# Performance work log

Hardware: AMD Instinct MI355X
Metric: run time of the kernel (lower is better)

## Reference

```python
import jax, jax.numpy as jnp
import numpy as np

E = 4      # num_ensemble
DIN = 256  # input_dim
D = 256    # d_model (output_dim)
B = 16
T = 1024
LN_EPS = 1e-5


def setup_inputs() -> dict:
    key = jax.random.key(0)
    ks = jax.random.split(key, 14)
    s = 0.02
    x = jax.random.normal(ks[0], (B, T, DIN), dtype=jnp.float32)
    in_proj_w = s * jax.random.normal(ks[1], (3, E, DIN, D), dtype=jnp.float32)
    in_proj_b = jnp.zeros((3, E, D), dtype=jnp.float32)
    mid_w = s * jax.random.normal(ks[2], (2, E, D, D), dtype=jnp.float32)
    mid_b = jnp.zeros((2, E, D), dtype=jnp.float32)
    ff_w1 = s * jax.random.normal(ks[3], (E, D, D), dtype=jnp.float32)
    ff_b1 = jnp.zeros((E, D), dtype=jnp.float32)
    ff_w2 = s * jax.random.normal(ks[4], (E, D, D), dtype=jnp.float32)
    ff_b2 = jnp.zeros((E, D), dtype=jnp.float32)
    ln_w = jnp.ones((E, D), dtype=jnp.float32)
    ln_b = jnp.zeros((E, D), dtype=jnp.float32)
    # LRU initializer (r_min=0.9, r_max=0.999)
    r_min, r_max = 0.9, 0.999
    u1 = jax.random.uniform(ks[5], (E, D), dtype=jnp.float32)
    u2 = jax.random.uniform(ks[6], (E, D), dtype=jnp.float32)
    nu_log = jnp.log(-0.5 * jnp.log(u1 * (r_max ** 2 - r_min ** 2) + r_min ** 2))
    theta_log = jnp.log(u2 * 2.0 * np.pi)
    # |lambda|^2 = exp(-2*exp(nu_log))
    gamma_log = jnp.log(jnp.sqrt(1.0 - jnp.exp(-2.0 * jnp.exp(nu_log))))
    params_log = jnp.stack([nu_log, theta_log, gamma_log], axis=0)  # (3,E,D)
    return {"x": x, "in_proj_w": in_proj_w, "in_proj_b": in_proj_b,
            "params_log": params_log, "mid_w": mid_w, "mid_b": mid_b,
            "ff_w1": ff_w1, "ff_b1": ff_b1, "ff_w2": ff_w2, "ff_b2": ff_b2,
            "ln_w": ln_w, "ln_b": ln_b}


def _forward(x, in_proj_w, in_proj_b, params_log, mid_w, mid_b,
             ff_w1, ff_b1, ff_w2, ff_b2, ln_w, ln_b):
    # in_proj: 3 ensemble linears -> u: (3, E, B, T, D)
    u = jnp.einsum('bti,keio->kebto', x, in_proj_w) + in_proj_b[:, :, None, None, :]
    input_real, input_imag, o = u[0], u[1], u[2]

    params = jnp.exp(params_log)           # (3,E,D)
    nu, theta, gamma = params[0], params[1], params[2]
    mag = jnp.exp(-nu)
    f_real = mag * jnp.cos(theta)          # (E,D)
    f_imag = mag * jnp.sin(theta)

    ir = gamma[:, None, None, :] * input_real  # (E,B,T,D)
    ii = gamma[:, None, None, :] * input_imag

    # complex linear recurrence h_t = f * h_{t-1} + u_t over time axis
    fr = f_real[:, None, :]                # (E,1,D) broadcast over B
    fi = f_imag[:, None, :]
    ir_t = jnp.moveaxis(ir, 2, 0)          # (T,E,B,D)
    ii_t = jnp.moveaxis(ii, 2, 0)

    def step(carry, ut):
        hr, hi = carry
        ur, ui = ut
        hr2 = fr * hr - fi * hi + ur
        hi2 = fr * hi + fi * hr + ui
        return (hr2, hi2), (hr2, hi2)

    h0 = (jnp.zeros((E, B, D), x.dtype), jnp.zeros((E, B, D), x.dtype))
    (hr_last, hi_last), (out_r_t, out_i_t) = jax.lax.scan(step, h0, (ir_t, ii_t))
    output_real = jnp.moveaxis(out_r_t, 0, 2)  # (E,B,T,D)
    output_imag = jnp.moveaxis(out_i_t, 0, 2)

    # hidden packing: (1, B, 2*E*D) with ensemble blocks concatenated, real then imag
    hr_pack = jnp.transpose(hr_last, (1, 0, 2)).reshape(B, E * D)
    hi_pack = jnp.transpose(hi_last, (1, 0, 2)).reshape(B, E * D)
    hidden = jnp.concatenate([hr_pack, hi_pack], axis=-1)[None]  # (1,B,2ED)

    # middle_proj: 2 ensemble linears applied to (real, imag)
    stacked = jnp.stack([output_real, output_imag], axis=0)  # (2,E,B,T,D)
    mid = jnp.einsum('kebtd,kedo->kebto', stacked, mid_w) + mid_b[:, :, None, None, :]
    out = mid[0] - mid[1] + o                                # (E,B,T,D)

    # EnsemblePositionWiseFeedForward (dropout=0 -> identity)
    h1 = jax.nn.gelu(jnp.einsum('ebtd,edo->ebto', out, ff_w1)
                     + ff_b1[:, None, None, :], approximate=False)
    h2 = jnp.einsum('ebtd,edo->ebto', h1, ff_w2) + ff_b2[:, None, None, :] + out
    # LayerNorm over joint (E, D) dims for each (b, t)
    mean = jnp.mean(h2, axis=(0, 3), keepdims=True)
    var = jnp.var(h2, axis=(0, 3), keepdims=True)
    out_ln = (h2 - mean) / jnp.sqrt(var + LN_EPS)
    out_ln = out_ln * ln_w[:, None, None, :] + ln_b[:, None, None, :]
    return out_ln, hidden


def reference(x, in_proj_w, in_proj_b, params_log, mid_w, mid_b,
              ff_w1, ff_b1, ff_w2, ff_b2, ln_w, ln_b):
    return _forward(x, in_proj_w, in_proj_b, params_log, mid_w, mid_b,
                    ff_w1, ff_b1, ff_w2, ff_b2, ln_w, ln_b)
```

## Files before the change

### kernel.cpp

```cpp
#include <hip/hip_runtime.h>
#include <stdint.h>

#define BT_ 16384
#define TT  1024
#define CHUNKS 32
#define CLEN   32
#define LANES  16384

typedef __bf16 bf16x8 __attribute__((ext_vector_type(8)));
typedef float  f32x4  __attribute__((ext_vector_type(4)));
typedef unsigned int u32x4 __attribute__((ext_vector_type(4)));
typedef unsigned short u16;

__device__ __forceinline__ float b2f(u16 s){
    union { float f; unsigned int u; } c; c.u = ((unsigned int)s) << 16; return c.f;
}
__device__ __forceinline__ u16 f2b(float f){
    union { float f; unsigned int u; } c; c.f = f;
    unsigned int u = c.u;
    return (u16)((u + 0x7fffu + ((u >> 16) & 1u)) >> 16);
}

__device__ __forceinline__ void gload_lds16(const u16* g, u16* lds){
    __builtin_amdgcn_global_load_lds(
        (const __attribute__((address_space(1))) void*)g,
        (__attribute__((address_space(3))) void*)lds, 16, 0, 0);
}

__global__ __launch_bounds__(256) void conv_k(const float* __restrict__ x, u16* __restrict__ xc)
{
    long i = ((long)blockIdx.x * 256 + threadIdx.x) * 8;
    float4 v0 = *reinterpret_cast<const float4*>(x + i);
    float4 v1 = *reinterpret_cast<const float4*>(x + i + 4);
    union { u16 s[8]; u32x4 v; } p;
    p.s[0] = f2b(v0.x); p.s[1] = f2b(v0.y); p.s[2] = f2b(v0.z); p.s[3] = f2b(v0.w);
    p.s[4] = f2b(v1.x); p.s[5] = f2b(v1.y); p.s[6] = f2b(v1.z); p.s[7] = f2b(v1.w);
    *reinterpret_cast<u32x4*>(xc + i) = p.v;
}

__global__ __launch_bounds__(256) void prep_w(
    const float* __restrict__ ipw, const float* __restrict__ mw,
    const float* __restrict__ fw1, const float* __restrict__ fw2,
    u16* __restrict__ d_ipw, u16* __restrict__ d_mw,
    u16* __restrict__ d_fw1, u16* __restrict__ d_fw2)
{
    __shared__ u16 tile[64][72];
    int blk = blockIdx.x;
    int w = blk >> 4, t = blk & 15;
    int tr = (t >> 2) * 64;
    int tc = (t & 3) * 64;
    const float* src; u16* dst; int ostride; float sign = 1.f;
    if (w < 12)      { src = ipw + (size_t)w * 65536; dst = d_ipw + (size_t)w * 65536; ostride = 256; }
    else if (w < 20) { int u = w - 12, c = u >> 2, e = u & 3;
                       src = mw + (size_t)u * 65536;
                       dst = d_mw + (size_t)e * 131072 + c * 256; ostride = 512;
                       if (c) sign = -1.f; }
    else if (w < 24) { int e = w - 20; src = fw1 + (size_t)e * 65536; dst = d_fw1 + (size_t)e * 65536; ostride = 256; }
    else             { int e = w - 24; src = fw2 + (size_t)e * 65536; dst = d_fw2 + (size_t)e * 65536; ostride = 256; }

    int q = threadIdx.x;
    int r = q >> 2, cb = (q & 3) * 16;
#pragma unroll
    for (int j = 0; j < 4; j++) {
        int col = cb + j * 4;
        const float4 v = *reinterpret_cast<const float4*>(src + (size_t)(tr + r) * 256 + tc + col);
        tile[r][col + 0] = f2b(v.x * sign);
        tile[r][col + 1] = f2b(v.y * sign);
        tile[r][col + 2] = f2b(v.z * sign);
        tile[r][col + 3] = f2b(v.w * sign);
    }
    __syncthreads();
    int ol = q >> 2, ib = (q & 3) * 16;
    union { u16 s[8]; u32x4 v; } p0, p1;
#pragma unroll
    for (int k = 0; k < 8; k++) { p0.s[k] = tile[ib + k][ol]; p1.s[k] = tile[ib + 8 + k][ol]; }
    u16* drow = dst + (size_t)(tc + ol) * ostride + tr + ib;
    *reinterpret_cast<u32x4*>(drow)     = p0.v;
    *reinterpret_cast<u32x4*>(drow + 8) = p1.v;
}

__global__ __launch_bounds__(256, 3) void gemm_k(
    const u16* __restrict__ A0, const u16* __restrict__ B0,
    const float* __restrict__ biasf, const u16* __restrict__ aux,
    const float* __restrict__ gamlogf, u16* __restrict__ out0,
    u16* __restrict__ out1, int K, int mode, int MT)
{
    __shared__ __align__(16) u16 Bs[64 * 256];
    __shared__ __align__(16) float fs_all[4][1024];

    int tid  = threadIdx.x;
    int wave = tid >> 6, lane = tid & 63;
    int quad = lane >> 4, l16 = lane & 15;
    int n0 = blockIdx.y * 64;
    int z = blockIdx.z;
    int e, k3 = 0;
    const u16* A;
    const u16* Bm;
    if (mode == 1) { k3 = z >> 2; e = z & 3; A = A0; }
    else           { e = z; A = A0 + (size_t)e * BT_ * K; }
    Bm = B0 + (size_t)(mode == 1 ? z : e) * 256 * K;

    int srow = lane >> 5, schunk = lane & 31;
    int nhalf = K >> 8;

    float bias_nf[4], gam_nf[4];
#pragma unroll
    for (int nf = 0; nf < 4; nf++) {
        int col = n0 + nf * 16 + l16;
        if (mode == 1) {
            bias_nf[nf] = biasf[z * 256 + col];
            gam_nf[nf] = (k3 < 2) ? expf(gamlogf[2048 + e * 256 + col]) : 1.f;
        } else if (mode == 2) {
            bias_nf[nf] = biasf[e * 256 + col] - biasf[1024 + e * 256 + col];
        } else {
            bias_nf[nf] = biasf[e * 256 + col];
        }
    }

    float* fs = fs_all[wave];
    int rr = lane >> 3, ch = lane & 7;

    for (int mt = 0; mt < MT; mt++) {
        int m0 = (blockIdx.x * MT + mt) * 256;

        f32x4 acc[4][4];
#pragma unroll
        for (int i = 0; i < 4; i++)
#pragma unroll
            for (int j = 0; j < 4; j++) acc[i][j] = (f32x4){0.f, 0.f, 0.f, 0.f};

        for (int kh = 0; kh < nhalf; kh++) {
            if (nhalf > 1 || mt == 0) {
                if (mt || kh) __syncthreads();
#pragma unroll
                for (int i = 0; i < 8; i++) {
                    int row = wave * 16 + i * 2 + srow;
                    int c = schunk ^ (row & 7);
                    gload_lds16(Bm + (size_t)(n0 + row) * K + kh * 256 + c * 8,
                                &Bs[(wave * 16 + i * 2) * 256]);
                }
                __syncthreads();
            }

            const u16* Ar0 = A + (size_t)(m0 + wave * 64 + l16) * K + kh * 256 + quad * 8;
            const u16* Ar1 = Ar0 + (size_t)16 * K;
            const u16* Ar2 = Ar0 + (size_t)32 * K;
            const u16* Ar3 = Ar0 + (size_t)48 * K;

            bf16x8 ac0, ac1, ac2, ac3, an0, an1, an2, an3;
            { union { u32x4 v; bf16x8 b; } u;
              u.v = *reinterpret_cast<const u32x4*>(Ar0); ac0 = u.b;
              u.v = *reinterpret_cast<const u32x4*>(Ar1); ac1 = u.b;
              u.v = *reinterpret_cast<const u32x4*>(Ar2); ac2 = u.b;
              u.v = *reinterpret_cast<const u32x4*>(Ar3); ac3 = u.b; }
#pragma unroll
            for (int kt = 0; kt < 8; kt++) {
                if (kt < 7) {
                    union { u32x4 v; bf16x8 b; } u;
                    u.v = *reinterpret_cast<const u32x4*>(Ar0 + (kt + 1) * 32); an0 = u.b;
                    u.v = *reinterpret_cast<const u32x4*>(Ar1 + (kt + 1) * 32); an1 = u.b;
                    u.v = *reinterpret_cast<const u32x4*>(Ar2 + (kt + 1) * 32); an2 = u.b;
                    u.v = *reinterpret_cast<const u32x4*>(Ar3 + (kt + 1) * 32); an3 = u.b;
                }
#pragma unroll
                for (int nf = 0; nf < 4; nf++) {
                    int row = nf * 16 + l16;
                    int c = (kt * 4 + quad) ^ (row & 7);
                    union { u32x4 v; bf16x8 b; } u;
                    u.v = *reinterpret_cast<const u32x4*>(&Bs[row * 256 + c * 8]);
                    acc[0][nf] = __builtin_amdgcn_mfma_f32_16x16x32_bf16(ac0, u.b, acc[0][nf], 0, 0, 0);
                    acc[1][nf] = __builtin_amdgcn_mfma_f32_16x16x32_bf16(ac1, u.b, acc[1][nf], 0, 0, 0);
                    acc[2][nf] = __builtin_amdgcn_mfma_f32_16x16x32_bf16(ac2, u.b, acc[2][nf], 0, 0, 0);
                    acc[3][nf] = __builtin_amdgcn_mfma_f32_16x16x32_bf16(ac3, u.b, acc[3][nf], 0, 0, 0);
                }
                ac0 = an0; ac1 = an1; ac2 = an2; ac3 = an3;
            }
        }

#pragma unroll
        for (int s = 0; s < 4; s++) {
#pragma unroll
            for (int nf = 0; nf < 4; nf++) {
                int colsw = (nf * 16 + l16) ^ (quad * 8);
#pragma unroll
                for (int r = 0; r < 4; r++) {
                    float v = acc[s][nf][r] + bias_nf[nf];
                    if (mode == 1) v *= gam_nf[nf];
                    if (mode == 3) v = 0.5f * v * (1.0f + erff(v * 0.70710678118654752f));
                    fs[(quad * 4 + r) * 64 + colsw] = v;
                }
            }
#pragma unroll
            for (int i = 0; i < 2; i++) {
                int rl = i * 8 + rr;
                int grow = m0 + wave * 64 + s * 16 + rl;
                const float* sp = fs + rl * 64 + ((ch * 8) ^ ((rl >> 2) * 8));
                f32x4 v0 = *reinterpret_cast<const f32x4*>(sp);
                f32x4 v1 = *reinterpret_cast<const f32x4*>(sp + 4);
                float w[8] = { v0[0], v0[1], v0[2], v0[3], v1[0], v1[1], v1[2], v1[3] };
                u16* dstp;
                if (mode == 1) {
                    if (k3 < 2) dstp = out0 + (((size_t)(e * BT_ + grow)) * 2 + k3) * 256 + n0 + ch * 8;
                    else        dstp = out1 + ((size_t)e * BT_ + grow) * 256 + n0 + ch * 8;
                } else {
                    dstp = out0 + ((size_t)e * BT_ + grow) * 256 + n0 + ch * 8;
                }
                if (mode == 2 || mode == 4) {
                    const u16* ap = aux + ((size_t)e * BT_ + grow) * 256 + n0 + ch * 8;
                    u32x4 av = *reinterpret_cast<const u32x4*>(ap);
#pragma unroll
                    for (int j = 0; j < 4; j++) {
                        w[2 * j]     += b2f((u16)(av[j] & 0xffffu));
                        w[2 * j + 1] += b2f((u16)(av[j] >> 16));
                    }
                }
                union { u16 s[8]; u32x4 v; } p;
#pragma unroll
                for (int j = 0; j < 8; j++) p.s[j] = f2b(w[j]);
                *reinterpret_cast<u32x4*>(dstp) = p.v;
            }
        }
    }
}

__global__ __launch_bounds__(256) void scan_a(const u16* __restrict__ u,
    const float* __restrict__ plog, float2* __restrict__ carry)
{
    int l2 = blockIdx.x * 256 + threadIdx.x;
    int chunk = blockIdx.y;
    int dd = (l2 & 127) * 2, b = (l2 >> 7) & 15, e = l2 >> 11;
    float nu0 = expf(plog[e * 256 + dd]),        nu1 = expf(plog[e * 256 + dd + 1]);
    float th0 = expf(plog[1024 + e * 256 + dd]), th1 = expf(plog[1024 + e * 256 + dd + 1]);
    float m0 = expf(-nu0), m1 = expf(-nu1);
    float fr0 = m0 * cosf(th0), fi0 = m0 * sinf(th0);
    float fr1 = m1 * cosf(th1), fi1 = m1 * sinf(th1);
    size_t base = ((size_t)e * BT_ + b * TT) * 512 + (size_t)chunk * CLEN * 512 + dd;
    float hr0 = 0.f, hi0 = 0.f, hr1 = 0.f, hi1 = 0.f;
    for (int t = 0; t < CLEN; t++) {
        unsigned int wr = *reinterpret_cast<const unsigned int*>(u + base);
        unsigned int wi = *reinterpret_cast<const unsigned int*>(u + base + 256);
        float ur0 = b2f((u16)wr), ur1 = b2f((u16)(wr >> 16));
        float ui0 = b2f((u16)wi), ui1 = b2f((u16)(wi >> 16));
        float a0 = fr0 * hr0 - fi0 * hi0 + ur0;
        float b0 = fr0 * hi0 + fi0 * hr0 + ui0;
        float a1 = fr1 * hr1 - fi1 * hi1 + ur1;
        float b1 = fr1 * hi1 + fi1 * hr1 + ui1;
        hr0 = a0; hi0 = b0; hr1 = a1; hi1 = b1;
        base += 512;
    }
    size_t ci = (size_t)chunk * LANES + (size_t)e * 4096 + b * 256 + dd;
    *reinterpret_cast<float4*>(&carry[ci]) = make_float4(hr0, hi0, hr1, hi1);
}

__global__ __launch_bounds__(256) void scan_b(const float* __restrict__ plog,
                                              float2* __restrict__ carry)
{
    int l = blockIdx.x * 256 + threadIdx.x;
    int d = l & 255, e = l >> 12;
    float nu = expf(plog[e * 256 + d]);
    float th = expf(plog[1024 + e * 256 + d]);
    float magL = expf(-nu * (float)CLEN);
    float ang = th * (float)CLEN;
    float frL = magL * cosf(ang), fiL = magL * sinf(ang);
    float gr = 0.f, gi = 0.f;
    for (int j = 0; j < CHUNKS; j++) {
        float2 c = carry[(size_t)j * LANES + l];
        carry[(size_t)j * LANES + l] = make_float2(gr, gi);
        float gr2 = frL * gr - fiL * gi + c.x;
        float gi2 = frL * gi + fiL * gr + c.y;
        gr = gr2; gi = gi2;
    }
}

__global__ __launch_bounds__(256) void scan_c(u16* __restrict__ u,
    const float* __restrict__ plog, const float2* __restrict__ carry,
    float* __restrict__ outh)
{
    int l2 = blockIdx.x * 256 + threadIdx.x;
    int chunk = blockIdx.y;
    int dd = (l2 & 127) * 2, b = (l2 >> 7) & 15, e = l2 >> 11;
    float nu0 = expf(plog[e * 256 + dd]),        nu1 = expf(plog[e * 256 + dd + 1]);
    float th0 = expf(plog[1024 + e * 256 + dd]), th1 = expf(plog[1024 + e * 256 + dd + 1]);
    float m0 = expf(-nu0), m1 = expf(-nu1);
    float fr0 = m0 * cosf(th0), fi0 = m0 * sinf(th0);
    float fr1 = m1 * cosf(th1), fi1 = m1 * sinf(th1);
    size_t base = ((size_t)e * BT_ + b * TT) * 512 + (size_t)chunk * CLEN * 512 + dd;
    size_t ci = (size_t)chunk * LANES + (size_t)e * 4096 + b * 256 + dd;
    float4 c0 = *reinterpret_cast<const float4*>(&carry[ci]);
    float hr0 = c0.x, hi0 = c0.y, hr1 = c0.z, hi1 = c0.w;
    for (int t = 0; t < CLEN; t++) {
        unsigned int wr = *reinterpret_cast<const unsigned int*>(u + base);
        unsigned int wi = *reinterpret_cast<const unsigned int*>(u + base + 256);
        float ur0 = b2f((u16)wr), ur1 = b2f((u16)(wr >> 16));
        float ui0 = b2f((u16)wi), ui1 = b2f((u16)(wi >> 16));
        float a0 = fr0 * hr0 - fi0 * hi0 + ur0;
        float b0 = fr0 * hi0 + fi0 * hr0 + ui0;
        float a1 = fr1 * hr1 - fi1 * hi1 + ur1;
        float b1 = fr1 * hi1 + fi1 * hr1 + ui1;
        hr0 = a0; hi0 = b0; hr1 = a1; hi1 = b1;
        *reinterpret_cast<unsigned int*>(u + base) =
            (unsigned int)f2b(hr0) | ((unsigned int)f2b(hr1) << 16);
        *reinterpret_cast<unsigned int*>(u + base + 256) =
            (unsigned int)f2b(hi0) | ((unsigned int)f2b(hi1) << 16);
        base += 512;
    }
    if (chunk == CHUNKS - 1) {
        float* oh = outh + (size_t)4 * BT_ * 256;
        *reinterpret_cast<float2*>(&oh[b * 2048 + e * 256 + dd])        = make_float2(hr0, hr1);
        *reinterpret_cast<float2*>(&oh[b * 2048 + 1024 + e * 256 + dd]) = make_float2(hi0, hi1);
    }
}

__global__ __launch_bounds__(256) void ln_k(const u16* __restrict__ h2,
    const float* __restrict__ lnw, const float* __restrict__ lnb,
    float* __restrict__ out)
{
    int r = blockIdx.x;
    int d = threadIdx.x;
    float v[4]; float s1 = 0.f, s2 = 0.f;
#pragma unroll
    for (int e = 0; e < 4; e++) {
        float x = b2f(h2[((size_t)e * BT_ + r) * 256 + d]);
        v[e] = x; s1 += x; s2 += x * x;
    }
#pragma unroll
    for (int off = 32; off; off >>= 1) {
        s1 += __shfl_down(s1, off, 64);
        s2 += __shfl_down(s2, off, 64);
    }
    __shared__ float sm[8];
    int wave = threadIdx.x >> 6, lane = threadIdx.x & 63;
    if (lane == 0) { sm[wave] = s1; sm[4 + wave] = s2; }
    __syncthreads();
    float S1 = sm[0] + sm[1] + sm[2] + sm[3];
    float S2 = sm[4] + sm[5] + sm[6] + sm[7];
    float mean = S1 * (1.0f / 1024.0f);
    float var = S2 * (1.0f / 1024.0f) - mean * mean;
    float rstd = rsqrtf(var + 1e-5f);
#pragma unroll
    for (int e = 0; e < 4; e++) {
        float o = (v[e] - mean) * rstd * lnw[e * 256 + d] + lnb[e * 256 + d];
        out[((size_t)e * BT_ + r) * 256 + d] = o;
    }
}

extern "C" void kernel_launch(void* const* d_in, const int* in_sizes, int n_in,
                              void* d_out, int out_size, void* d_ws, size_t ws_size,
                              hipStream_t stream)
{
    const float* x    = (const float*)d_in[0];
    const float* ipw  = (const float*)d_in[1];
    const float* ipb  = (const float*)d_in[2];
    const float* plog = (const float*)d_in[3];
    const float* mw   = (const float*)d_in[4];
    const float* mb   = (const float*)d_in[5];
    const float* fw1  = (const float*)d_in[6];
    const float* fb1  = (const float*)d_in[7];
    const float* fw2  = (const float*)d_in[8];
    const float* fb2  = (const float*)d_in[9];
    const float* lnw  = (const float*)d_in[10];
    const float* lnb  = (const float*)d_in[11];
    float* out = (float*)d_out;

    u16* W = (u16*)d_ws;
    u16* buf_u    = W;
    u16* buf_out  = W + (size_t)33554432;
    u16* xc       = W + (size_t)33554432;
    float2* carry = (float2*)(W + (size_t)37748736);
    u16* buf_mw_t = W + (size_t)50331648;
    u16* c_ipw_t  = W + (size_t)50855936;
    u16* c_fw1_t  = W + (size_t)51642368;
    u16* c_fw2_t  = W + (size_t)51904512;
    u16* scratch  = (u16*)d_out;

    conv_k<<<2048, 256, 0, stream>>>(x, xc);
    prep_w<<<448, 256, 0, stream>>>(ipw, mw, fw1, fw2, c_ipw_t, buf_mw_t, c_fw1_t, c_fw2_t);
    gemm_k<<<dim3(16, 4, 12), 256, 0, stream>>>(xc, c_ipw_t, ipb, nullptr, plog, buf_u, scratch, 256, 1, 4);
    scan_a<<<dim3(32, CHUNKS), 256, 0, stream>>>(buf_u, plog, carry);
    scan_b<<<64, 256, 0, stream>>>(plog, carry);
    scan_c<<<dim3(32, CHUNKS), 256, 0, stream>>>(buf_u, plog, carry, out);
    gemm_k<<<dim3(32, 4, 4), 256, 0, stream>>>(buf_u, buf_mw_t, mb, scratch, nullptr, buf_out, nullptr, 512, 2, 2);
    gemm_k<<<dim3(32, 4, 4), 256, 0, stream>>>(buf_out, c_fw1_t, fb1, nullptr, nullptr, scratch, nullptr, 256, 3, 2);
    gemm_k<<<dim3(32, 4, 4), 256, 0, stream>>>(scratch, c_fw2_t, fb2, buf_out, nullptr, buf_u, nullptr, 256, 4, 2);
    ln_k<<<16384, 256, 0, stream>>>(buf_u, lnw, lnb, out);
}
```

Measured before the change: 319.5 us.

## Swap MFMA operands to write GEMM epilogue directly, drop LDS staging, raise occupancy

```diff
diff --git a/kernel.cpp b/kernel.cpp
--- a/kernel.cpp
+++ b/kernel.cpp
@@ -10,6 +10,7 @@
 typedef __bf16 bf16x8 __attribute__((ext_vector_type(8)));
 typedef float  f32x4  __attribute__((ext_vector_type(4)));
 typedef unsigned int u32x4 __attribute__((ext_vector_type(4)));
+typedef unsigned int u32x2 __attribute__((ext_vector_type(2)));
 typedef unsigned short u16;
 
 __device__ __forceinline__ float b2f(u16 s){
@@ -79,14 +80,13 @@
     *reinterpret_cast<u32x4*>(drow + 8) = p1.v;
 }
 
-__global__ __launch_bounds__(256, 3) void gemm_k(
+__global__ __launch_bounds__(256, 4) void gemm_k(
     const u16* __restrict__ A0, const u16* __restrict__ B0,
     const float* __restrict__ biasf, const u16* __restrict__ aux,
     const float* __restrict__ gamlogf, u16* __restrict__ out0,
     u16* __restrict__ out1, int K, int mode, int MT)
 {
     __shared__ __align__(16) u16 Bs[64 * 256];
-    __shared__ __align__(16) float fs_all[4][1024];
 
     int tid  = threadIdx.x;
     int wave = tid >> 6, lane = tid & 63;
@@ -103,23 +103,6 @@
     int srow = lane >> 5, schunk = lane & 31;
     int nhalf = K >> 8;
 
-    float bias_nf[4], gam_nf[4];
-#pragma unroll
-    for (int nf = 0; nf < 4; nf++) {
-        int col = n0 + nf * 16 + l16;
-        if (mode == 1) {
-            bias_nf[nf] = biasf[z * 256 + col];
-            gam_nf[nf] = (k3 < 2) ? expf(gamlogf[2048 + e * 256 + col]) : 1.f;
-        } else if (mode == 2) {
-            bias_nf[nf] = biasf[e * 256 + col] - biasf[1024 + e * 256 + col];
-        } else {
-            bias_nf[nf] = biasf[e * 256 + col];
-        }
-    }
-
-    float* fs = fs_all[wave];
-    int rr = lane >> 3, ch = lane & 7;
-
     for (int mt = 0; mt < MT; mt++) {
         int m0 = (blockIdx.x * MT + mt) * 256;
 
@@ -168,56 +151,64 @@
                     int c = (kt * 4 + quad) ^ (row & 7);
                     union { u32x4 v; bf16x8 b; } u;
                     u.v = *reinterpret_cast<const u32x4*>(&Bs[row * 256 + c * 8]);
-                    acc[0][nf] = __builtin_amdgcn_mfma_f32_16x16x32_bf16(ac0, u.b, acc[0][nf], 0, 0, 0);
-                    acc[1][nf] = __builtin_amdgcn_mfma_f32_16x16x32_bf16(ac1, u.b, acc[1][nf], 0, 0, 0);
-                    acc[2][nf] = __builtin_amdgcn_mfma_f32_16x16x32_bf16(ac2, u.b, acc[2][nf], 0, 0, 0);
-                    acc[3][nf] = __builtin_amdgcn_mfma_f32_16x16x32_bf16(ac3, u.b, acc[3][nf], 0, 0, 0);
+                    acc[0][nf] = __builtin_amdgcn_mfma_f32_16x16x32_bf16(u.b, ac0, acc[0][nf], 0, 0, 0);
+                    acc[1][nf] = __builtin_amdgcn_mfma_f32_16x16x32_bf16(u.b, ac1, acc[1][nf], 0, 0, 0);
+                    acc[2][nf] = __builtin_amdgcn_mfma_f32_16x16x32_bf16(u.b, ac2, acc[2][nf], 0, 0, 0);
+                    acc[3][nf] = __builtin_amdgcn_mfma_f32_16x16x32_bf16(u.b, ac3, acc[3][nf], 0, 0, 0);
                 }
                 ac0 = an0; ac1 = an1; ac2 = an2; ac3 = an3;
             }
         }
 
+        float bias_c[4][4], gam_c[4][4];
+#pragma unroll
+        for (int nf = 0; nf < 4; nf++)
+#pragma unroll
+            for (int r = 0; r < 4; r++) {
+                int col = n0 + nf * 16 + quad * 4 + r;
+                if (mode == 1) {
+                    bias_c[nf][r] = biasf[z * 256 + col];
+                    gam_c[nf][r] = (k3 < 2) ? expf(gamlogf[2048 + e * 256 + col]) : 1.f;
+                } else if (mode == 2) {
+                    bias_c[nf][r] = biasf[e * 256 + col] - biasf[1024 + e * 256 + col];
+                } else {
+                    bias_c[nf][r] = biasf[e * 256 + col];
+                }
+            }
+
 #pragma unroll
         for (int s = 0; s < 4; s++) {
+            int grow = m0 + wave * 64 + s * 16 + l16;
 #pragma unroll
             for (int nf = 0; nf < 4; nf++) {
-                int colsw = (nf * 16 + l16) ^ (quad * 8);
+                float w[4];
 #pragma unroll
                 for (int r = 0; r < 4; r++) {
-                    float v = acc[s][nf][r] + bias_nf[nf];
-                    if (mode == 1) v *= gam_nf[nf];
+                    float v = acc[s][nf][r] + bias_c[nf][r];
+                    if (mode == 1) v *= gam_c[nf][r];
                     if (mode == 3) v = 0.5f * v * (1.0f + erff(v * 0.70710678118654752f));
-                    fs[(quad * 4 + r) * 64 + colsw] = v;
-                }
-            }
-#pragma unroll
-            for (int i = 0; i < 2; i++) {
-                int rl = i * 8 + rr;
-                int grow = m0 + wave * 64 + s * 16 + rl;
-                const float* sp = fs + rl * 64 + ((ch * 8) ^ ((rl >> 2) * 8));
-                f32x4 v0 = *reinterpret_cast<const f32x4*>(sp);
-                f32x4 v1 = *reinterpret_cast<const f32x4*>(sp + 4);
-                float w[8] = { v0[0], v0[1], v0[2], v0[3], v1[0], v1[1], v1[2], v1[3] };
+                    w[r] = v;
+                }
+                int colb = n0 + nf * 16 + quad * 4;
                 u16* dstp;
                 if (mode == 1) {
-                    if (k3 < 2) dstp = out0 + (((size_t)(e * BT_ + grow)) * 2 + k3) * 256 + n0 + ch * 8;
-                    else        dstp = out1 + ((size_t)e * BT_ + grow) * 256 + n0 + ch * 8;
+                    if (k3 < 2) dstp = out0 + (((size_t)(e * BT_ + grow)) * 2 + k3) * 256 + colb;
+                    else        dstp = out1 + ((size_t)e * BT_ + grow) * 256 + colb;
                 } else {
-                    dstp = out0 + ((size_t)e * BT_ + grow) * 256 + n0 + ch * 8;
+                    dstp = out0 + ((size_t)e * BT_ + grow) * 256 + colb;
                 }
                 if (mode == 2 || mode == 4) {
-                    const u16* ap = aux + ((size_t)e * BT_ + grow) * 256 + n0 + ch * 8;
-                    u32x4 av = *reinterpret_cast<const u32x4*>(ap);
-#pragma unroll
-                    for (int j = 0; j < 4; j++) {
-                        w[2 * j]     += b2f((u16)(av[j] & 0xffffu));
-                        w[2 * j + 1] += b2f((u16)(av[j] >> 16));
-                    }
-                }
-                union { u16 s[8]; u32x4 v; } p;
-#pragma unroll
-                for (int j = 0; j < 8; j++) p.s[j] = f2b(w[j]);
-                *reinterpret_cast<u32x4*>(dstp) = p.v;
+                    const u16* ap = aux + ((size_t)e * BT_ + grow) * 256 + colb;
+                    u32x2 av = *reinterpret_cast<const u32x2*>(ap);
+                    w[0] += b2f((u16)(av[0] & 0xffffu));
+                    w[1] += b2f((u16)(av[0] >> 16));
+                    w[2] += b2f((u16)(av[1] & 0xffffu));
+                    w[3] += b2f((u16)(av[1] >> 16));
+                }
+                u32x2 pv;
+                pv[0] = (unsigned int)f2b(w[0]) | ((unsigned int)f2b(w[1]) << 16);
+                pv[1] = (unsigned int)f2b(w[2]) | ((unsigned int)f2b(w[3]) << 16);
+                *reinterpret_cast<u32x2*>(dstp) = pv;
             }
         }
     }
@@ -375,12 +366,12 @@
 
     conv_k<<<2048, 256, 0, stream>>>(x, xc);
     prep_w<<<448, 256, 0, stream>>>(ipw, mw, fw1, fw2, c_ipw_t, buf_mw_t, c_fw1_t, c_fw2_t);
-    gemm_k<<<dim3(16, 4, 12), 256, 0, stream>>>(xc, c_ipw_t, ipb, nullptr, plog, buf_u, scratch, 256, 1, 4);
+    gemm_k<<<dim3(32, 4, 12), 256, 0, stream>>>(xc, c_ipw_t, ipb, nullptr, plog, buf_u, scratch, 256, 1, 2);
     scan_a<<<dim3(32, CHUNKS), 256, 0, stream>>>(buf_u, plog, carry);
     scan_b<<<64, 256, 0, stream>>>(plog, carry);
     scan_c<<<dim3(32, CHUNKS), 256, 0, stream>>>(buf_u, plog, carry, out);
-    gemm_k<<<dim3(32, 4, 4), 256, 0, stream>>>(buf_u, buf_mw_t, mb, scratch, nullptr, buf_out, nullptr, 512, 2, 2);
-    gemm_k<<<dim3(32, 4, 4), 256, 0, stream>>>(buf_out, c_fw1_t, fb1, nullptr, nullptr, scratch, nullptr, 256, 3, 2);
-    gemm_k<<<dim3(32, 4, 4), 256, 0, stream>>>(scratch, c_fw2_t, fb2, buf_out, nullptr, buf_u, nullptr, 256, 4, 2);
+    gemm_k<<<dim3(64, 4, 4), 256, 0, stream>>>(buf_u, buf_mw_t, mb, scratch, nullptr, buf_out, nullptr, 512, 2, 1);
+    gemm_k<<<dim3(64, 4, 4), 256, 0, stream>>>(buf_out, c_fw1_t, fb1, nullptr, nullptr, scratch, nullptr, 256, 3, 1);
+    gemm_k<<<dim3(64, 4, 4), 256, 0, stream>>>(scratch, c_fw2_t, fb2, buf_out, nullptr, buf_u, nullptr, 256, 4, 1);
     ln_k<<<16384, 256, 0, stream>>>(buf_u, lnw, lnb, out);
 }
```

Result: slower. 631.2 us (+97.5%).
